# Kernel optimization log

Hardware: AMD Instinct MI355X
Metric: run time of the kernel (lower is better)

The kernel has to match this reference:

```python
import jax, jax.numpy as jnp
import numpy as np

N_NODES = 100000
N_EDGES = 3200000
N_GRAPHS = 64
IN_DIM, OUT_DIM = 16, 3


def _gcn_layer(x, src, dst, ew, W, b, n):
    # PyG GCNConv with edge_weight: transform first, then normalized propagate
    # with added self-loops (weight 1.0). deg_i = sum_{e: dst=i} w_e + 1.
    xw = x @ W  # [N, out]
    deg = jax.ops.segment_sum(ew, dst, num_segments=n) + 1.0  # [N]
    dinv = jax.lax.rsqrt(deg)
    norm = dinv[src] * ew * dinv[dst]  # [E]
    agg = jax.ops.segment_sum(xw[src] * norm[:, None], dst, num_segments=n)
    # self-loop contribution: dinv_i * 1.0 * dinv_i = 1/deg_i
    return agg + xw * (1.0 / deg)[:, None] + b


def setup_inputs() -> dict:
    key = jax.random.key(0)
    ks = jax.random.split(key, 16)
    glorot = lambda k, fi, fo: jax.random.normal(k, (fi, fo), jnp.float32) * jnp.sqrt(2.0 / (fi + fo))
    return {
        "x": jax.random.normal(ks[0], (N_NODES, IN_DIM), jnp.float32),
        "edge_index": jax.random.randint(ks[1], (2, N_EDGES), 0, N_NODES, jnp.int32),
        "edge_attr": jax.random.uniform(ks[2], (N_EDGES,), jnp.float32),
        "batch": jnp.sort(jax.random.randint(ks[3], (N_NODES,), 0, N_GRAPHS, jnp.int32)),
        "W1": glorot(ks[4], IN_DIM, 16), "b1": jnp.zeros((16,), jnp.float32),
        "W2": glorot(ks[5], 16, 64),     "b2": jnp.zeros((64,), jnp.float32),
        "W3": glorot(ks[6], 64, 256),    "b3": jnp.zeros((256,), jnp.float32),
        "L1": glorot(ks[7], 256, 128),   "c1": jnp.zeros((128,), jnp.float32),
        "L2": glorot(ks[8], 128, 64),    "c2": jnp.zeros((64,), jnp.float32),
        "L3": glorot(ks[9], 64, OUT_DIM), "c3": jnp.zeros((OUT_DIM,), jnp.float32),
    }


def reference(x, edge_index, edge_attr, batch, W1, b1, W2, b2, W3, b3, L1, c1, L2, c2, L3, c3):
    src, dst = edge_index[0], edge_index[1]
    h = jax.nn.silu(_gcn_layer(x, src, dst, edge_attr, W1, b1, N_NODES))
    h = jax.nn.silu(_gcn_layer(h, src, dst, edge_attr, W2, b2, N_NODES))
    h = jax.nn.silu(_gcn_layer(h, src, dst, edge_attr, W3, b3, N_NODES))
    # global mean pool per graph
    sums = jax.ops.segment_sum(h, batch, num_segments=N_GRAPHS)  # [G, 256]
    cnt = jax.ops.segment_sum(jnp.ones((N_NODES,), h.dtype), batch, num_segments=N_GRAPHS)
    pooled = sums / jnp.maximum(cnt, 1.0)[:, None]
    z = jax.nn.silu(pooled @ L1 + c1)
    z = jax.nn.silu(z @ L2 + c2)
    z = z @ L3 + c3
    return jnp.squeeze(z)
```

## Files before the change

### kernel.cpp

```cpp
#include <hip/hip_runtime.h>
#include <math.h>


#define NBH 1024
#define POOL_C 8
#define CAP 10240

typedef _Float16 half8 __attribute__((ext_vector_type(8)));
typedef float f32x4 __attribute__((ext_vector_type(4)));

__device__ __forceinline__ float silu_f(float v) { return v / (1.0f + expf(-v)); }

__device__ __forceinline__ int psrc(unsigned u) { return (int)(u >> 15); }
__device__ __forceinline__ float pew(unsigned u) {
    unsigned short hs = (unsigned short)(u & 0x7FFFu);
    _Float16 hv;
    __builtin_memcpy(&hv, &hs, 2);
    return (float)hv;
}
__device__ __forceinline__ unsigned packent(int src, float w) {
    _Float16 hw = (_Float16)w;
    unsigned short hb;
    __builtin_memcpy(&hb, &hw, 2);
    return ((unsigned)src << 15) | (unsigned)(hb & 0x7FFFu);
}

__global__ void k_init(const int* __restrict__ batch, int* __restrict__ bounds,
                       int* __restrict__ btotal, int N, int G) {
    int t = threadIdx.x;
    btotal[t] = 0;
    if (t > G) return;
    if (t == G) { bounds[G] = N; return; }
    int lo = 0, hi = N;
    while (lo < hi) { int m = (lo + hi) >> 1; if (batch[m] < t) lo = m + 1; else hi = m; }
    bounds[t] = lo;
}

__global__ __launch_bounds__(256) void k_bscatter(const int* __restrict__ src,
                                                  const int* __restrict__ dst,
                                                  const float* __restrict__ ew,
                                                  int* __restrict__ btotal,
                                                  int2* __restrict__ ebuf,
                                                  int E, int B, int ept) {
    __shared__ int hist[512];
    __shared__ int cur[512];
    int blk = blockIdx.x, t = threadIdx.x;
    for (int i = t; i < B; i += 256) hist[i] = 0;
    __syncthreads();
    int start = blk * 256 * ept;
    for (int j = 0; j < ept; j++) {
        int e = start + j * 256 + t;
        if (e < E) atomicAdd(&hist[dst[e] >> 8], 1);
    }
    __syncthreads();
    for (int b = t; b < B; b += 256)
        cur[b] = b * CAP + atomicAdd(&btotal[b], hist[b]);
    __syncthreads();
    for (int j = 0; j < ept; j++) {
        int e = start + j * 256 + t;
        if (e < E) {
            int d = dst[e];
            int b = d >> 8;
            int pos = atomicAdd(&cur[b], 1);
            if (pos < (b + 1) * CAP)
                ebuf[pos] = make_int2(src[e] | ((d & 255) << 24), __float_as_int(ew[e]));
        }
    }
}

__global__ __launch_bounds__(256) void k_bucket_csr(const int2* __restrict__ ebuf,
                                                    const int* __restrict__ btotal,
                                                    unsigned int* __restrict__ csr,
                                                    unsigned int* __restrict__ offs,
                                                    float* __restrict__ dinv,
                                                    const float* __restrict__ x,
                                                    _Float16* __restrict__ xp,
                                                    int N) {
    __shared__ int ncnt[256];
    __shared__ int excl[256];
    __shared__ float wsum[256];
    int b = blockIdx.x, t = threadIdx.x;
    int base = b * CAP;
    int end = base + min(btotal[b], CAP);
    ncnt[t] = 0;
    wsum[t] = 0.0f;
    __syncthreads();
    for (int i = base + t; i < end; i += 256)
        atomicAdd(&ncnt[(unsigned)ebuf[i].x >> 24], 1);
    __syncthreads();
    int v = ncnt[t];
    excl[t] = v;
    __syncthreads();
#pragma unroll
    for (int o = 1; o < 256; o <<= 1) {
        int x2 = (t >= o) ? excl[t - o] : 0;
        __syncthreads();
        excl[t] += x2;
        __syncthreads();
    }
    int ex = excl[t] - v;
    int n = (b << 8) + t;
    if (n < N) offs[n] = (unsigned)(base + ex) | ((unsigned)v << 24);
    __syncthreads();
    ncnt[t] = base + ex;
    __syncthreads();
    for (int i = base + t; i < end; i += 256) {
        int2 ent = ebuf[i];
        int node = (unsigned)ent.x >> 24;
        float w = __int_as_float(ent.y);
        int pos = atomicAdd(&ncnt[node], 1);
        csr[pos] = packent(ent.x & 0x00FFFFFF, w);
        atomicAdd(&wsum[node], w);
    }
    __syncthreads();
    if (n < N) {
        float dv = 1.0f / sqrtf(1.0f + wsum[t]);
        dinv[n] = dv;
        const float4* xr = (const float4*)(x + (long long)n * 16);
        half8* xw = (half8*)(xp + (long long)n * 16);
#pragma unroll
        for (int j = 0; j < 2; j++) {
            float4 a = xr[2 * j], c = xr[2 * j + 1];
            half8 hv;
            hv[0] = (_Float16)(a.x * dv); hv[1] = (_Float16)(a.y * dv);
            hv[2] = (_Float16)(a.z * dv); hv[3] = (_Float16)(a.w * dv);
            hv[4] = (_Float16)(c.x * dv); hv[5] = (_Float16)(c.y * dv);
            hv[6] = (_Float16)(c.z * dv); hv[7] = (_Float16)(c.w * dv);
            xw[j] = hv;
        }
    }
}

__global__ __launch_bounds__(256) void k_gx1(const _Float16* __restrict__ h,
                                             const unsigned int* __restrict__ csr,
                                             const unsigned int* __restrict__ offs,
                                             const float* __restrict__ dinv,
                                             const float* __restrict__ W,
                                             const float* __restrict__ b,
                                             _Float16* __restrict__ out, int N) {
    __shared__ float Ws[16 * 16];
    __shared__ float bs[16];
    if (threadIdx.x < 256) Ws[threadIdx.x] = W[threadIdx.x];
    if (threadIdx.x < 16) bs[threadIdx.x] = b[threadIdx.x];
    __syncthreads();
    int n = blockIdx.x * 4 + (threadIdx.x >> 6);
    n = __builtin_amdgcn_readfirstlane(n);
    if (n >= N) return;
    int lane = threadIdx.x & 63;
    int d = lane & 15, eg = lane >> 4;
    unsigned op = offs[n];
    int p0 = op & 0x00FFFFFF;
    int len = op >> 24;
    int qs = p0 + ((len * eg) >> 2);
    int qe = p0 + ((len * (eg + 1)) >> 2);
    float acc = 0.0f;
    int p = qs;
    for (; p + 7 < qe; p += 8) {
        unsigned ee[8];
#pragma unroll
        for (int i = 0; i < 8; i++) ee[i] = csr[p + i];
        float vv[8];
#pragma unroll
        for (int i = 0; i < 8; i++) vv[i] = (float)h[psrc(ee[i]) * 16 + d];
#pragma unroll
        for (int i = 0; i < 8; i++) acc += pew(ee[i]) * vv[i];
    }
    if (p + 3 < qe) {
        unsigned e0 = csr[p], e1 = csr[p + 1], e2 = csr[p + 2], e3 = csr[p + 3];
        float v0 = (float)h[psrc(e0) * 16 + d], v1 = (float)h[psrc(e1) * 16 + d];
        float v2 = (float)h[psrc(e2) * 16 + d], v3 = (float)h[psrc(e3) * 16 + d];
        acc += pew(e0) * v0; acc += pew(e1) * v1;
        acc += pew(e2) * v2; acc += pew(e3) * v3;
        p += 4;
    }
    if (p + 1 < qe) {
        unsigned e0 = csr[p], e1 = csr[p + 1];
        acc += pew(e0) * (float)h[psrc(e0) * 16 + d];
        acc += pew(e1) * (float)h[psrc(e1) * 16 + d];
        p += 2;
    }
    if (p < qe) {
        unsigned e0 = csr[p];
        acc += pew(e0) * (float)h[psrc(e0) * 16 + d];
    }
    acc += __shfl_down(acc, 32, 64);
    acc += __shfl_down(acc, 16, 64);
    float dv = dinv[n];
    float yv = (acc + ((lane < 16) ? (float)h[n * 16 + lane] : 0.0f)) * dv;
    float o = bs[d];
#pragma unroll
    for (int k = 0; k < 16; k++) o += __shfl(yv, k, 64) * Ws[k * 16 + d];
    if (lane < 16) out[n * 16 + lane] = (_Float16)(silu_f(o) * dv);
}

__global__ __launch_bounds__(256) void k_gx2(const _Float16* __restrict__ h,
                                             const unsigned int* __restrict__ csr,
                                             const unsigned int* __restrict__ offs,
                                             const float* __restrict__ dinv,
                                             const float* __restrict__ W,
                                             const float* __restrict__ b,
                                             _Float16* __restrict__ out, int N) {
    __shared__ float Ws[16 * 64];
    __shared__ float bs[64];
    for (int i = threadIdx.x; i < 16 * 64; i += 256) Ws[i] = W[i];
    if (threadIdx.x < 64) bs[threadIdx.x] = b[threadIdx.x];
    __syncthreads();
    int n = blockIdx.x * 4 + (threadIdx.x >> 6);
    n = __builtin_amdgcn_readfirstlane(n);
    if (n >= N) return;
    int lane = threadIdx.x & 63;
    int d = lane & 15, eg = lane >> 4;
    unsigned op = offs[n];
    int p0 = op & 0x00FFFFFF;
    int len = op >> 24;
    int qs = p0 + ((len * eg) >> 2);
    int qe = p0 + ((len * (eg + 1)) >> 2);
    float acc = 0.0f;
    int p = qs;
    for (; p + 7 < qe; p += 8) {
        unsigned ee[8];
#pragma unroll
        for (int i = 0; i < 8; i++) ee[i] = csr[p + i];
        float vv[8];
#pragma unroll
        for (int i = 0; i < 8; i++) vv[i] = (float)h[psrc(ee[i]) * 16 + d];
#pragma unroll
        for (int i = 0; i < 8; i++) acc += pew(ee[i]) * vv[i];
    }
    if (p + 3 < qe) {
        unsigned e0 = csr[p], e1 = csr[p + 1], e2 = csr[p + 2], e3 = csr[p + 3];
        float v0 = (float)h[psrc(e0) * 16 + d], v1 = (float)h[psrc(e1) * 16 + d];
        float v2 = (float)h[psrc(e2) * 16 + d], v3 = (float)h[psrc(e3) * 16 + d];
        acc += pew(e0) * v0; acc += pew(e1) * v1;
        acc += pew(e2) * v2; acc += pew(e3) * v3;
        p += 4;
    }
    if (p + 1 < qe) {
        unsigned e0 = csr[p], e1 = csr[p + 1];
        acc += pew(e0) * (float)h[psrc(e0) * 16 + d];
        acc += pew(e1) * (float)h[psrc(e1) * 16 + d];
        p += 2;
    }
    if (p < qe) {
        unsigned e0 = csr[p];
        acc += pew(e0) * (float)h[psrc(e0) * 16 + d];
    }
    acc += __shfl_down(acc, 32, 64);
    acc += __shfl_down(acc, 16, 64);
    float dv = dinv[n];
    float yv = (acc + ((lane < 16) ? (float)h[n * 16 + lane] : 0.0f)) * dv;
    float o = bs[lane];
#pragma unroll
    for (int k = 0; k < 16; k++) o += __shfl(yv, k, 64) * Ws[k * 64 + lane];
    out[(long long)n * 64 + lane] = (_Float16)(silu_f(o) * dv);
}

__global__ __launch_bounds__(256) void k_gather64(const _Float16* __restrict__ h,
                                                  const unsigned int* __restrict__ csr,
                                                  const unsigned int* __restrict__ offs,
                                                  const float* __restrict__ dinv,
                                                  _Float16* __restrict__ y, int N) {
    int n = blockIdx.x * 4 + (threadIdx.x >> 6);
    n = __builtin_amdgcn_readfirstlane(n);
    if (n >= N) return;
    int lane = threadIdx.x & 63;
    unsigned op = offs[n];
    const unsigned* row = csr + (op & 0x00FFFFFF);
    int len = op >> 24;
    float acc = 0.0f;
    int j = 0;
    for (; j + 7 < len; j += 8) {
        unsigned ee[8];
        float vv[8];
#pragma unroll
        for (int i = 0; i < 8; i++) ee[i] = row[j + i];
#pragma unroll
        for (int i = 0; i < 8; i++) vv[i] = (float)h[psrc(ee[i]) * 64 + lane];
#pragma unroll
        for (int i = 0; i < 8; i++) acc += pew(ee[i]) * vv[i];
    }
    if (j + 3 < len) {
        unsigned e0 = row[j], e1 = row[j + 1], e2 = row[j + 2], e3 = row[j + 3];
        float v0 = (float)h[psrc(e0) * 64 + lane];
        float v1 = (float)h[psrc(e1) * 64 + lane];
        float v2 = (float)h[psrc(e2) * 64 + lane];
        float v3 = (float)h[psrc(e3) * 64 + lane];
        acc += pew(e0) * v0;
        acc += pew(e1) * v1;
        acc += pew(e2) * v2;
        acc += pew(e3) * v3;
        j += 4;
    }
    for (; j < len; j++) {
        unsigned e0 = row[j];
        acc += pew(e0) * (float)h[psrc(e0) * 64 + lane];
    }
    y[n * 64 + lane] = (_Float16)((acc + (float)h[n * 64 + lane]) * dinv[n]);
}

__global__ __launch_bounds__(256) void k_xform3pool(const _Float16* __restrict__ y,
                                                    const float* __restrict__ W,
                                                    const float* __restrict__ b,
                                                    const int* __restrict__ bounds,
                                                    float* __restrict__ partial,
                                                    int N) {
    int lane = threadIdx.x & 63;
    int wave = threadIdx.x >> 6;
    int g = blockIdx.x / POOL_C;
    int c = blockIdx.x % POOL_C;
    int s = bounds[g], e = bounds[g + 1];
    int len = e - s;
    int cs = s + (int)((long long)len * c / POOL_C);
    int ce = s + (int)((long long)len * (c + 1) / POOL_C);
    int lg = lane >> 4;
    int lr = lane & 15;

    half8 bf[4][2];
#pragma unroll
    for (int t = 0; t < 4; t++) {
        int col = (wave * 4 + t) * 16 + lr;
#pragma unroll
        for (int s2 = 0; s2 < 2; s2++) {
            half8 v;
#pragma unroll
            for (int j = 0; j < 8; j++)
                v[j] = (_Float16)W[(s2 * 32 + lg * 8 + j) * 256 + col];
            bf[t][s2] = v;
        }
    }
    float bias[4];
#pragma unroll
    for (int t = 0; t < 4; t++) bias[t] = b[(wave * 4 + t) * 16 + lr];

    float pacc[4] = {0.f, 0.f, 0.f, 0.f};

    for (int base = cs; base < ce; base += 16) {
        int node = base + lr;
        int cn = node < N ? node : N - 1;
        const half8* arow = (const half8*)(y + (long long)cn * 64);
        half8 a0 = arow[lg];
        half8 a1 = arow[4 + lg];
#pragma unroll
        for (int t = 0; t < 4; t++) {
            f32x4 acc = {0.f, 0.f, 0.f, 0.f};
            acc = __builtin_amdgcn_mfma_f32_16x16x32_f16(a0, bf[t][0], acc, 0, 0, 0);
            acc = __builtin_amdgcn_mfma_f32_16x16x32_f16(a1, bf[t][1], acc, 0, 0, 0);
#pragma unroll
            for (int r = 0; r < 4; r++) {
                int nrow = base + lg * 4 + r;
                if (nrow < ce) pacc[t] += silu_f(acc[r] + bias[t]);
            }
        }
    }
#pragma unroll
    for (int t = 0; t < 4; t++) {
        pacc[t] += __shfl_xor(pacc[t], 16, 64);
        pacc[t] += __shfl_xor(pacc[t], 32, 64);
    }
    if (lane < 16) {
        float* pr = partial + (long long)blockIdx.x * 256 + wave * 64;
#pragma unroll
        for (int t = 0; t < 4; t++) pr[t * 16 + lane] = pacc[t];
    }
}

__global__ __launch_bounds__(256) void k_mlp(const float* __restrict__ partial,
                                             const int* __restrict__ bounds,
                                             const float* __restrict__ L1,
                                             const float* __restrict__ c1,
                                             const float* __restrict__ L2,
                                             const float* __restrict__ c2,
                                             const float* __restrict__ L3,
                                             const float* __restrict__ c3,
                                             float* __restrict__ out) {
    __shared__ float pooled[256];
    __shared__ float z1[128];
    __shared__ float z2[64];
    int g = blockIdx.x;
    int t = threadIdx.x;
    int cnt = bounds[g + 1] - bounds[g];
    float s = 0.0f;
    for (int c = 0; c < POOL_C; c++) s += partial[((long long)g * POOL_C + c) * 256 + t];
    pooled[t] = s / (float)(cnt > 0 ? cnt : 1);
    __syncthreads();
    if (t < 128) {
        float acc = c1[t];
        for (int k = 0; k < 256; k++) acc += pooled[k] * L1[k * 128 + t];
        z1[t] = silu_f(acc);
    }
    __syncthreads();
    if (t < 64) {
        float acc = c2[t];
        for (int k = 0; k < 128; k++) acc += z1[k] * L2[k * 64 + t];
        z2[t] = silu_f(acc);
    }
    __syncthreads();
    if (t < 3) {
        float acc = c3[t];
        for (int k = 0; k < 64; k++) acc += z2[k] * L3[k * 3 + t];
        out[g * 3 + t] = acc;
    }
}

extern "C" void kernel_launch(void* const* d_in, const int* in_sizes, int n_in,
                              void* d_out, int out_size, void* d_ws, size_t ws_size,
                              hipStream_t stream) {
    const float* x     = (const float*)d_in[0];
    const int*   ei    = (const int*)d_in[1];
    const float* ea    = (const float*)d_in[2];
    const int*   batch = (const int*)d_in[3];
    const float* W1 = (const float*)d_in[4];
    const float* b1 = (const float*)d_in[5];
    const float* W2 = (const float*)d_in[6];
    const float* b2 = (const float*)d_in[7];
    const float* W3 = (const float*)d_in[8];
    const float* b3 = (const float*)d_in[9];
    const float* L1 = (const float*)d_in[10];
    const float* c1 = (const float*)d_in[11];
    const float* L2 = (const float*)d_in[12];
    const float* c2 = (const float*)d_in[13];
    const float* L3 = (const float*)d_in[14];
    const float* c3 = (const float*)d_in[15];
    float* out = (float*)d_out;

    const int N = in_sizes[0] / 16;
    const int E = in_sizes[2];
    const int G = out_size / 3;
    const int* src = ei;
    const int* dst = ei + E;
    const int B = (N + 255) >> 8;
    const int ept = (E + NBH * 256 - 1) / (NBH * 256);

    char* ws = (char*)d_ws;
    size_t off = 0;
    auto alloc = [&](size_t bytes) -> void* {
        void* p = (void*)(ws + off);
        off += (bytes + 255) & ~(size_t)255;
        return p;
    };
    float*        dinv    = (float*)alloc((size_t)N * 4);
    unsigned int* offs    = (unsigned int*)alloc((size_t)N * 4);
    int*          btotal  = (int*)  alloc(512 * 4);
    int*          bounds  = (int*)  alloc((size_t)(G + 1) * 4);
    int2*         ebuf    = (int2*) alloc((size_t)B * CAP * 8);
    unsigned int* csr     = (unsigned int*)alloc((size_t)B * CAP * 4);
    _Float16*     xp      = (_Float16*)alloc((size_t)N * 16 * 2);
    _Float16*     h1s     = (_Float16*)alloc((size_t)N * 16 * 2);
    _Float16*     h2s     = (_Float16*)alloc((size_t)N * 64 * 2);
    _Float16*     y64     = (_Float16*)alloc((size_t)N * 64 * 2);
    float*        partial = (float*)alloc((size_t)G * POOL_C * 256 * 4);
    (void)ws_size;

    k_init<<<1, 512, 0, stream>>>(batch, bounds, btotal, N, G);
    k_bscatter<<<NBH, 256, 0, stream>>>(src, dst, ea, btotal, ebuf, E, B, ept);
    k_bucket_csr<<<B, 256, 0, stream>>>(ebuf, btotal, csr, offs, dinv, x, xp, N);

    k_gx1<<<(N + 3) / 4, 256, 0, stream>>>(xp, csr, offs, dinv, W1, b1, h1s, N);

    k_gx2<<<(N + 3) / 4, 256, 0, stream>>>(h1s, csr, offs, dinv, W2, b2, h2s, N);

    k_gather64<<<(N + 3) / 4, 256, 0, stream>>>(h2s, csr, offs, dinv, y64, N);
    k_xform3pool<<<G * POOL_C, 256, 0, stream>>>(y64, W3, b3, bounds, partial, N);

    k_mlp<<<G, 256, 0, stream>>>(partial, bounds, L1, c1, L2, c2, L3, c3, out);
}
```

Before: 426.9 us.

## Stage bucket scatter through shared memory for contiguous global writes

The edge bucketing kernel now sorts each block's slice of edges by bucket in shared memory, using a block-wide prefix scan over the bucket histogram. It then writes them to the global bucket buffer in slice order, so consecutive threads write mostly contiguous runs within each bucket instead of scattered single entries. It also keeps dst in registers to avoid reloading it, and sizes the grid from a fixed 13 edges per thread. The cost is much more shared memory per block (about 33KB), which can lower occupancy, plus extra barriers for the scan.

Measured after the change: 396.8 us. -7.1%, faster.

```diff
diff --git a/kernel.cpp b/kernel.cpp
--- a/kernel.cpp
+++ b/kernel.cpp
@@ -2,7 +2,8 @@
 #include <math.h>
 
 
-#define NBH 1024
+#define EPT 13
+#define SLICE (256 * EPT)
 #define POOL_C 8
 #define CAP 10240
 
@@ -41,30 +42,75 @@
                                                   const float* __restrict__ ew,
                                                   int* __restrict__ btotal,
                                                   int2* __restrict__ ebuf,
-                                                  int E, int B, int ept) {
+                                                  int E, int B) {
     __shared__ int hist[512];
-    __shared__ int cur[512];
+    __shared__ int pscan[256];
+    __shared__ int excl[512];
+    __shared__ int hcur[512];
+    __shared__ int delta[512];
+    __shared__ int2 sbuf[SLICE];
+    __shared__ unsigned short bbk[SLICE];
     int blk = blockIdx.x, t = threadIdx.x;
-    for (int i = t; i < B; i += 256) hist[i] = 0;
-    __syncthreads();
-    int start = blk * 256 * ept;
-    for (int j = 0; j < ept; j++) {
+    int start = blk * SLICE;
+    int m = E - start;
+    if (m > SLICE) m = SLICE;
+    if (m < 0) m = 0;
+
+    for (int i = t; i < 512; i += 256) hist[i] = 0;
+    __syncthreads();
+
+    int dreg[EPT];
+#pragma unroll
+    for (int j = 0; j < EPT; j++) {
         int e = start + j * 256 + t;
-        if (e < E) atomicAdd(&hist[dst[e] >> 8], 1);
-    }
-    __syncthreads();
-    for (int b = t; b < B; b += 256)
-        cur[b] = b * CAP + atomicAdd(&btotal[b], hist[b]);
-    __syncthreads();
-    for (int j = 0; j < ept; j++) {
+        dreg[j] = (e < E) ? dst[e] : -1;
+        if (dreg[j] >= 0) atomicAdd(&hist[dreg[j] >> 8], 1);
+    }
+    __syncthreads();
+
+    int h0 = hist[2 * t], h1 = hist[2 * t + 1];
+    pscan[t] = h0 + h1;
+    __syncthreads();
+#pragma unroll
+    for (int o = 1; o < 256; o <<= 1) {
+        int x2 = (t >= o) ? pscan[t - o] : 0;
+        __syncthreads();
+        pscan[t] += x2;
+        __syncthreads();
+    }
+    int pex = pscan[t] - (h0 + h1);
+    excl[2 * t] = pex;
+    excl[2 * t + 1] = pex + h0;
+    hcur[2 * t] = pex;
+    hcur[2 * t + 1] = pex + h0;
+    __syncthreads();
+
+    for (int b = t; b < 512; b += 256) {
+        int cnt = hist[b];
+        int gb = b * CAP;
+        if (b < B && cnt > 0) gb += atomicAdd(&btotal[b], cnt);
+        delta[b] = gb - excl[b];
+    }
+    __syncthreads();
+
+#pragma unroll
+    for (int j = 0; j < EPT; j++) {
         int e = start + j * 256 + t;
         if (e < E) {
-            int d = dst[e];
+            int d = dreg[j];
             int b = d >> 8;
-            int pos = atomicAdd(&cur[b], 1);
-            if (pos < (b + 1) * CAP)
-                ebuf[pos] = make_int2(src[e] | ((d & 255) << 24), __float_as_int(ew[e]));
+            int pos = atomicAdd(&hcur[b], 1);
+            sbuf[pos] = make_int2(src[e] | ((d & 255) << 24), __float_as_int(ew[e]));
+            bbk[pos] = (unsigned short)b;
         }
+    }
+    __syncthreads();
+
+    for (int i = t; i < m; i += 256) {
+        int b = bbk[i];
+        int gpos = delta[b] + i;
+        if (gpos < (b + 1) * CAP)
+            ebuf[gpos] = sbuf[i];
     }
 }
 
@@ -429,7 +475,7 @@
     const int* src = ei;
     const int* dst = ei + E;
     const int B = (N + 255) >> 8;
-    const int ept = (E + NBH * 256 - 1) / (NBH * 256);
+    const int NBH = (E + SLICE - 1) / SLICE;
 
     char* ws = (char*)d_ws;
     size_t off = 0;
@@ -452,7 +498,7 @@
     (void)ws_size;
 
     k_init<<<1, 512, 0, stream>>>(batch, bounds, btotal, N, G);
-    k_bscatter<<<NBH, 256, 0, stream>>>(src, dst, ea, btotal, ebuf, E, B, ept);
+    k_bscatter<<<NBH, 256, 0, stream>>>(src, dst, ea, btotal, ebuf, E, B);
     k_bucket_csr<<<B, 256, 0, stream>>>(ebuf, btotal, csr, offs, dinv, x, xp, N);
 
     k_gx1<<<(N + 3) / 4, 256, 0, stream>>>(xp, csr, offs, dinv, W1, b1, h1s, N);
```
